# Kernel optimization log

Hardware: AMD Instinct MI355X
Metric: run time of the kernel (lower is better)

The kernel has to match this reference:

```python
import jax, jax.numpy as jnp
import numpy as np
import math

D_MODEL = 32    # channels; expand=1 => d_inner == d_model
D_STATE = 8
D_CONV = 4
DT_RANK = math.ceil(D_MODEL / 16)  # 2


def _layernorm(x, g, b, eps=1e-5):
    m = jnp.mean(x, axis=-1, keepdims=True)
    v = jnp.var(x, axis=-1, keepdims=True)
    return (x - m) * jax.lax.rsqrt(v + eps) * g + b


def _causal_dwconv(x, w, b):
    # x: [B, D, L], w: [D, 1, K] depthwise causal conv (pad K-1 on the left)
    y = jax.lax.conv_general_dilated(
        x, w, window_strides=(1,), padding=[(D_CONV - 1, 0)],
        dimension_numbers=('NCH', 'OIH', 'NCH'),
        feature_group_count=x.shape[1])
    return y + b[None, :, None]


def _ssm_branch(xb, z, conv_w, conv_b, xproj_w, dtproj_w, dtproj_b, A_log, Dp):
    # One mamba_inner (no out_proj) branch. xb, z: [B, D, L]
    Bsz, Dd, L = xb.shape
    u = jax.nn.silu(_causal_dwconv(xb, conv_w, conv_b))              # [B,D,L]
    x_dbl = jnp.einsum('bdl,rd->blr', u, xproj_w)                    # [B,L,R+2N]
    dt = x_dbl[..., :DT_RANK]                                        # [B,L,R]
    Bm = x_dbl[..., DT_RANK:DT_RANK + D_STATE]                       # [B,L,N]
    Cm = x_dbl[..., DT_RANK + D_STATE:]                              # [B,L,N]
    delta = jax.nn.softplus(jnp.einsum('blr,dr->bld', dt, dtproj_w) + dtproj_b)  # [B,L,D]
    A = -jnp.exp(A_log)                                              # [D,N]

    def step(h, inp):
        d_l, u_l, B_l, C_l = inp   # [B,D], [B,D], [B,N], [B,N]
        dA = jnp.exp(d_l[..., None] * A)                             # [B,D,N]
        h = dA * h + (d_l * u_l)[..., None] * B_l[:, None, :]
        y = jnp.einsum('bdn,bn->bd', h, C_l)
        return h, y

    h0 = jnp.zeros((Bsz, Dd, D_STATE), dtype=xb.dtype)
    _, ys = jax.lax.scan(step, h0,
                         (delta.transpose(1, 0, 2), u.transpose(2, 0, 1),
                          Bm.transpose(1, 0, 2), Cm.transpose(1, 0, 2)))
    y = ys.transpose(1, 2, 0)                                        # [B,D,L]
    y = y + Dp[None, :, None] * u
    return y * jax.nn.silu(z)


def _forward(x, w1, b1, ln_g, ln_b, in_proj_w,
             conv_w_f, conv_b_f, xproj_w_f, dtproj_w_f, dtproj_b_f, A_log_f, D_f,
             conv_w_b, conv_b_b, xproj_w_b, dtproj_w_b, dtproj_b_b, A_log_b, D_b,
             norm_g, norm_b, out_proj_w, w2, b2):
    s = jnp.max(x, axis=(2, 3))                                      # AdaptiveMaxPool2d((1,1)) -> [B,L]
    h = s[..., None] * w1[None, None, :, 0] + b1                     # Linear(1, d_model) -> [B,L,D]
    h = _layernorm(h, ln_g, ln_b)
    # Mamba, bimamba v2
    xz = jnp.einsum('bld,ed->bel', h, in_proj_w)                     # [B,2D,L]
    x_f, z_f = jnp.split(xz, 2, axis=1)
    out_f = _ssm_branch(x_f, z_f, conv_w_f, conv_b_f, xproj_w_f,
                        dtproj_w_f, dtproj_b_f, A_log_f, D_f)
    xz_r = jnp.flip(xz, axis=-1)
    x_b, z_b = jnp.split(xz_r, 2, axis=1)
    out_b = _ssm_branch(x_b, z_b, conv_w_b, conv_b_b, xproj_w_b,
                        dtproj_w_b, dtproj_b_b, A_log_b, D_b)
    y = (out_f + jnp.flip(out_b, axis=-1)).transpose(0, 2, 1)        # [B,L,D]
    y = _layernorm(y, norm_g, norm_b) / 2.0                          # use_norm + if_devide_out
    y = jnp.einsum('bld,od->blo', y, out_proj_w)                     # out_proj -> [B,L,D]
    o = jnp.einsum('bld,od->blo', y, w2) + b2                        # Linear(d_model, 1) -> [B,L,1]
    return jax.nn.sigmoid(o)[..., None]                              # [B,L,1,1]


def setup_inputs() -> dict:
    key = jax.random.key(0)
    ks = jax.random.split(key, 16)
    B, Cin, H, W = 16, 128, 256, 256
    D, N, R = D_MODEL, D_STATE, DT_RANK

    def nrm(k, shp, s=0.2):
        return jax.random.normal(k, shp, dtype=jnp.float32) * s

    A_log_init = jnp.log(jnp.arange(1, N + 1, dtype=jnp.float32))[None, :] * jnp.ones((D, 1), jnp.float32)
    return dict(
        x=jax.random.normal(ks[0], (B, Cin, H, W), dtype=jnp.float32),
        w1=nrm(ks[1], (D, 1), 0.5), b1=nrm(ks[2], (D,), 0.1),
        ln_g=jnp.ones((D,), jnp.float32), ln_b=jnp.zeros((D,), jnp.float32),
        in_proj_w=nrm(ks[3], (2 * D, D)),
        conv_w_f=nrm(ks[4], (D, 1, D_CONV)), conv_b_f=nrm(ks[5], (D,), 0.1),
        xproj_w_f=nrm(ks[6], (R + 2 * N, D)),
        dtproj_w_f=nrm(ks[7], (D, R)), dtproj_b_f=nrm(ks[8], (D,), 0.1),
        A_log_f=A_log_init, D_f=jnp.ones((D,), jnp.float32),
        conv_w_b=nrm(ks[9], (D, 1, D_CONV)), conv_b_b=nrm(ks[10], (D,), 0.1),
        xproj_w_b=nrm(ks[11], (R + 2 * N, D)),
        dtproj_w_b=nrm(ks[12], (D, R)), dtproj_b_b=nrm(ks[13], (D,), 0.1),
        A_log_b=A_log_init, D_b=jnp.ones((D,), jnp.float32),
        norm_g=jnp.ones((D,), jnp.float32), norm_b=jnp.zeros((D,), jnp.float32),
        out_proj_w=nrm(ks[14], (D, D)),
        w2=nrm(ks[15], (1, D), 0.5), b2=jnp.zeros((1,), jnp.float32),
    )


def reference(x, w1, b1, ln_g, ln_b, in_proj_w,
              conv_w_f, conv_b_f, xproj_w_f, dtproj_w_f, dtproj_b_f, A_log_f, D_f,
              conv_w_b, conv_b_b, xproj_w_b, dtproj_w_b, dtproj_b_b, A_log_b, D_b,
              norm_g, norm_b, out_proj_w, w2, b2):
    return _forward(x, w1, b1, ln_g, ln_b, in_proj_w,
                    conv_w_f, conv_b_f, xproj_w_f, dtproj_w_f, dtproj_b_f, A_log_f, D_f,
                    conv_w_b, conv_b_b, xproj_w_b, dtproj_w_b, dtproj_b_b, A_log_b, D_b,
                    norm_g, norm_b, out_proj_w, w2, b2)
```

## Files before the change

kernel.cpp:

```cpp
#include <hip/hip_runtime.h>
#include <hip/hip_bf16.h>
#include <math.h>

#define B_SZ 16
#define L_SEQ 128
#define D_M 32
#define HW 65536
#define NROWS (B_SZ * 128)
#define NCHUNK 2

typedef float vfloat4 __attribute__((ext_vector_type(4)));

__device__ float g_part[NROWS * NCHUNK];
__device__ float g_y[2][B_SZ * D_M * L_SEQ];
__device__ int   g_done[B_SZ];

__device__ __forceinline__ float silu_acc(float x) {
    return x / (1.f + __expf(-x));
}
__device__ __forceinline__ float softplusf(float x) {
    return (x > 20.f) ? x : log1pf(__expf(x));
}

__device__ __forceinline__ float row_max(int row) {
    const int r2 = row * NCHUNK;
    return fmaxf(g_part[r2], g_part[r2 + 1]);
}

__device__ __forceinline__ void compute_h(int row, const float* __restrict__ w1,
                                          const float* __restrict__ b1,
                                          const float* __restrict__ lng,
                                          const float* __restrict__ lnb,
                                          float h[D_M]) {
    const float s = row_max(row);
    float mean = 0.f;
#pragma unroll
    for (int d = 0; d < D_M; d++) { h[d] = s * w1[d] + b1[d]; mean += h[d]; }
    mean *= (1.f / D_M);
    float var = 0.f;
#pragma unroll
    for (int d = 0; d < D_M; d++) { float t = h[d] - mean; var += t * t; }
    var *= (1.f / D_M);
    const float rs = rsqrtf(var + 1e-5f);
#pragma unroll
    for (int d = 0; d < D_M; d++) h[d] = (h[d] - mean) * rs * lng[d] + lnb[d];
}

__global__ __launch_bounds__(256) void kmax(const float* __restrict__ x) {
    const int blk = blockIdx.x;
    const vfloat4* __restrict__ p =
        reinterpret_cast<const vfloat4*>(x) + (size_t)blk * 8192;
    const int t = threadIdx.x;
    float m0 = -INFINITY, m1 = -INFINITY, m2 = -INFINITY, m3 = -INFINITY;
#pragma unroll
    for (int i = 0; i < 8192; i += 1024) {
        vfloat4 v0 = __builtin_nontemporal_load(p + i + t);
        vfloat4 v1 = __builtin_nontemporal_load(p + i + t + 256);
        vfloat4 v2 = __builtin_nontemporal_load(p + i + t + 512);
        vfloat4 v3 = __builtin_nontemporal_load(p + i + t + 768);
        m0 = fmaxf(m0, fmaxf(fmaxf(v0.x, v0.y), fmaxf(v0.z, v0.w)));
        m1 = fmaxf(m1, fmaxf(fmaxf(v1.x, v1.y), fmaxf(v1.z, v1.w)));
        m2 = fmaxf(m2, fmaxf(fmaxf(v2.x, v2.y), fmaxf(v2.z, v2.w)));
        m3 = fmaxf(m3, fmaxf(fmaxf(v3.x, v3.y), fmaxf(v3.z, v3.w)));
    }
    float m = fmaxf(fmaxf(m0, m1), fmaxf(m2, m3));
#pragma unroll
    for (int off = 32; off >= 1; off >>= 1)
        m = fmaxf(m, __shfl_xor(m, off));
    __shared__ float sm[4];
    if ((threadIdx.x & 63) == 0) sm[threadIdx.x >> 6] = m;
    __syncthreads();
    if (threadIdx.x == 0)
        g_part[blk] = fmaxf(fmaxf(sm[0], sm[1]), fmaxf(sm[2], sm[3]));
}

__global__ __launch_bounds__(1024) void ktail(
    const float* __restrict__ w1,  const float* __restrict__ b1,
    const float* __restrict__ lng, const float* __restrict__ lnb,
    const float* __restrict__ Win,
    const float* __restrict__ cw_f, const float* __restrict__ cb_f,
    const float* __restrict__ xp_f, const float* __restrict__ dtw_f,
    const float* __restrict__ dtb_f, const float* __restrict__ Al_f,
    const float* __restrict__ Dp_f,
    const float* __restrict__ cw_b, const float* __restrict__ cb_b,
    const float* __restrict__ xp_b, const float* __restrict__ dtw_b,
    const float* __restrict__ dtb_b, const float* __restrict__ Al_b,
    const float* __restrict__ Dp_b,
    const float* __restrict__ ng,  const float* __restrict__ nb,
    const float* __restrict__ Wout, const float* __restrict__ w2,
    const float* __restrict__ b2,  float* __restrict__ out) {
    const int b   = blockIdx.x >> 1;
    const int dir = blockIdx.x & 1;
    const int tid = threadIdx.x;

    const float* cw  = dir ? cw_b  : cw_f;
    const float* cb  = dir ? cb_b  : cb_f;
    const float* xp  = dir ? xp_b  : xp_f;
    const float* dtw = dir ? dtw_b : dtw_f;
    const float* dtb = dir ? dtb_b : dtb_f;
    const float* Al  = dir ? Al_b  : Al_f;
    const float* Dp  = dir ? Dp_b  : Dp_f;

    __shared__ __align__(16) float S[15136];
    __shared__ int s_flag;
    float* sx  = S;
    float* sdl = S;
    float* su  = S + 4352;
    float* sy  = S + 8576;
    float* sdt = S + 12800;
    float* sB  = S + 13056;
    float* sC  = S + 14080;
    float* smm = S + 15104;

    const int l = tid & 127;
    const int q = tid >> 7;
    const int qq = __builtin_amdgcn_readfirstlane(q);

    if (tid < 128) sx[(tid >> 2) * 136 + (tid & 3)] = 0.f;
    if (tid >= 128 && tid < 160) {
        const int d = tid - 128;
        float mm = 0.f;
#pragma unroll
        for (int o = 0; o < D_M; o++) mm += w2[o] * Wout[o * 32 + d];
        smm[d] = mm;
    }
    float h[D_M];
    compute_h(b * L_SEQ + l, w1, b1, lng, lnb, h);

    {
        const int lw = dir ? (127 - l) : l;
#pragma unroll
        for (int k = 0; k < 4; k++) {
            const int e = qq * 4 + k;
            float acc = 0.f;
#pragma unroll
            for (int d = 0; d < D_M; d++) acc += h[d] * Win[e * 32 + d];
            sx[e * 136 + 4 + lw] = acc;
        }
    }

    float zs[4];
#pragma unroll
    for (int k = 0; k < 4; k++) {
        const int d = qq * 4 + k;
        float z = 0.f;
#pragma unroll
        for (int kk = 0; kk < D_M; kk++) z += h[kk] * Win[(32 + d) * 32 + kk];
        zs[k] = silu_acc(z);
    }
    __syncthreads();

    {
        const int d  = tid >> 5;
        const int l0 = (tid & 31) * 4;
        const vfloat4* px = reinterpret_cast<const vfloat4*>(sx + d * 136 + l0);
        vfloat4 a0 = px[0], a1 = px[1];
        float xv[7] = {a0.y, a0.z, a0.w, a1.x, a1.y, a1.z, a1.w};
        const float c0 = cw[d*4+0], c1 = cw[d*4+1], c2 = cw[d*4+2], c3 = cw[d*4+3];
        const float cbd = cb[d];
        float uo[4];
#pragma unroll
        for (int j = 0; j < 4; j++) {
            float acc = cbd + c0*xv[j] + c1*xv[j+1] + c2*xv[j+2] + c3*xv[j+3];
            uo[j] = silu_acc(acc);
        }
        vfloat4 u0 = {uo[0], uo[1], uo[2], uo[3]};
        *reinterpret_cast<vfloat4*>(su + d * 132 + l0) = u0;
    }
    __syncthreads();

    {
        float ul[D_M];
#pragma unroll
        for (int d = 0; d < D_M; d++) ul[d] = su[d * 132 + l];
#pragma unroll
        for (int rep = 0; rep < 3; rep++) {
            const int r = qq + rep * 8;
            if (rep == 2 && qq >= 2) break;
            float acc = 0.f;
#pragma unroll
            for (int d = 0; d < D_M; d++) acc += ul[d] * xp[r * 32 + d];
            if (r < 2)       sdt[l * 2 + r] = acc;
            else if (r < 10) sB[l * 8 + (r - 2)] = acc;
            else             sC[l * 8 + (r - 10)] = acc;
        }
    }
    __syncthreads();

    {
        const float dt0 = sdt[l * 2 + 0], dt1 = sdt[l * 2 + 1];
        const int d0 = qq * 4;
#pragma unroll
        for (int j = 0; j < 4; j++) {
            const int d = d0 + j;
            const float t = dt0 * dtw[d * 2 + 0] + dt1 * dtw[d * 2 + 1] + dtb[d];
            sdl[l * 33 + d] = softplusf(t);
        }
    }
    __syncthreads();

    if (tid < 256) {
        const int d = tid >> 3;
        const int c = tid & 7;
        float An[8];
        {
            const vfloat4* ap = reinterpret_cast<const vfloat4*>(Al + d * 8);
            vfloat4 a0 = ap[0], a1 = ap[1];
            An[0]=a0.x; An[1]=a0.y; An[2]=a0.z; An[3]=a0.w;
            An[4]=a1.x; An[5]=a1.y; An[6]=a1.z; An[7]=a1.w;
#pragma unroll
            for (int n = 0; n < 8; n++) An[n] = -__expf(An[n]);
        }
        const float Dd = Dp[d];
        const int lbase = c * 16;

        float Ap[8], Wp[8];
#pragma unroll
        for (int n = 0; n < 8; n++) { Ap[n] = 1.f; Wp[n] = 0.f; }
        for (int i = 0; i < 16; i++) {
            const int ll = lbase + i;
            const float dl = sdl[ll * 33 + d];
            const float ul = su[d * 132 + ll];
            const float du = dl * ul;
            const vfloat4* bp = reinterpret_cast<const vfloat4*>(sB + ll * 8);
            vfloat4 b0 = bp[0], b1 = bp[1];
            float Bv[8] = {b0.x,b0.y,b0.z,b0.w,b1.x,b1.y,b1.z,b1.w};
#pragma unroll
            for (int n = 0; n < 8; n++) {
                const float dA = __expf(dl * An[n]);
                Wp[n] = dA * Wp[n] + du * Bv[n];
                Ap[n] *= dA;
            }
        }
#pragma unroll
        for (int s = 1; s < 8; s <<= 1) {
#pragma unroll
            for (int n = 0; n < 8; n++) {
                const float Au = __shfl_up(Ap[n], s, 8);
                const float Wu = __shfl_up(Wp[n], s, 8);
                if (c >= s) {
                    Wp[n] = Ap[n] * Wu + Wp[n];
                    Ap[n] = Ap[n] * Au;
                }
            }
        }
        float hn[8];
#pragma unroll
        for (int n = 0; n < 8; n++) {
            const float Wu = __shfl_up(Wp[n], 1, 8);
            hn[n] = (c == 0) ? 0.f : Wu;
        }
        for (int i = 0; i < 16; i++) {
            const int ll = lbase + i;
            const float dl = sdl[ll * 33 + d];
            const float ul = su[d * 132 + ll];
            const float du = dl * ul;
            const vfloat4* bp = reinterpret_cast<const vfloat4*>(sB + ll * 8);
            const vfloat4* cp = reinterpret_cast<const vfloat4*>(sC + ll * 8);
            vfloat4 b0 = bp[0], b1 = bp[1];
            vfloat4 c0 = cp[0], c1 = cp[1];
            float Bv[8] = {b0.x,b0.y,b0.z,b0.w,b1.x,b1.y,b1.z,b1.w};
            float Cv[8] = {c0.x,c0.y,c0.z,c0.w,c1.x,c1.y,c1.z,c1.w};
            float y = 0.f;
#pragma unroll
            for (int n = 0; n < 8; n++) {
                const float dA = __expf(dl * An[n]);
                hn[n] = dA * hn[n] + du * Bv[n];
                y += hn[n] * Cv[n];
            }
            sy[d * 132 + ll] = y + Dd * ul;
        }
    }
    __syncthreads();

    for (int i = tid; i < 4096; i += 1024) {
        const int d = i >> 7, li = i & 127;
        const int gl = dir ? (127 - li) : li;
        g_y[dir][(b * D_M + d) * L_SEQ + gl] = sy[d * 132 + li];
    }
    __syncthreads();

    if (tid == 0) {
        __threadfence();
        const int old = atomicAdd(&g_done[b], 1);
        const int win = (old == 1);
        if (win) {
            atomicExch(&g_done[b], 0);
            __threadfence();
        }
        s_flag = win;
    }
    __syncthreads();
    if (!s_flag) return;

    {
        float* sv = S;
        const float* y0 = g_y[0] + (size_t)b * D_M * L_SEQ;
        const float* y1 = g_y[1] + (size_t)b * D_M * L_SEQ;

#pragma unroll
        for (int k = 0; k < 4; k++) {
            const int d = qq * 4 + k;
            const float yc = y0[d * L_SEQ + l] + y1[d * L_SEQ + l];
            sv[l * 33 + d] = yc * zs[k];
        }
        __syncthreads();

        if (tid < 128) {
            float vv[D_M];
            float mean = 0.f;
#pragma unroll
            for (int d = 0; d < D_M; d++) { vv[d] = sv[l * 33 + d]; mean += vv[d]; }
            mean *= (1.f / D_M);
            float var = 0.f;
#pragma unroll
            for (int d = 0; d < D_M; d++) { float t = vv[d] - mean; var += t * t; }
            var *= (1.f / D_M);
            const float rs = rsqrtf(var + 1e-5f);

            float acc = b2[0];
#pragma unroll
            for (int d = 0; d < D_M; d++) {
                const float y = ((vv[d] - mean) * rs * ng[d] + nb[d]) * 0.5f;
                acc += y * smm[d];
            }
            out[b * L_SEQ + l] = 1.f / (1.f + __expf(-acc));
        }
    }
}

extern "C" void kernel_launch(void* const* d_in, const int* in_sizes, int n_in,
                              void* d_out, int out_size, void* d_ws, size_t ws_size,
                              hipStream_t stream) {
    const float* x        = (const float*)d_in[0];
    const float* w1       = (const float*)d_in[1];
    const float* b1       = (const float*)d_in[2];
    const float* ln_g     = (const float*)d_in[3];
    const float* ln_b     = (const float*)d_in[4];
    const float* in_proj  = (const float*)d_in[5];
    const float* cw_f     = (const float*)d_in[6];
    const float* cb_f     = (const float*)d_in[7];
    const float* xp_f     = (const float*)d_in[8];
    const float* dtw_f    = (const float*)d_in[9];
    const float* dtb_f    = (const float*)d_in[10];
    const float* Al_f     = (const float*)d_in[11];
    const float* Dp_f     = (const float*)d_in[12];
    const float* cw_b     = (const float*)d_in[13];
    const float* cb_b     = (const float*)d_in[14];
    const float* xp_b     = (const float*)d_in[15];
    const float* dtw_b    = (const float*)d_in[16];
    const float* dtb_b    = (const float*)d_in[17];
    const float* Al_b     = (const float*)d_in[18];
    const float* Dp_b     = (const float*)d_in[19];
    const float* norm_g   = (const float*)d_in[20];
    const float* norm_b   = (const float*)d_in[21];
    const float* Wout     = (const float*)d_in[22];
    const float* w2       = (const float*)d_in[23];
    const float* b2       = (const float*)d_in[24];

    kmax<<<NROWS * NCHUNK, 256, 0, stream>>>(x);
    ktail<<<B_SZ * 2, 1024, 0, stream>>>(w1, b1, ln_g, ln_b, in_proj,
                                         cw_f, cb_f, xp_f, dtw_f, dtb_f, Al_f, Dp_f,
                                         cw_b, cb_b, xp_b, dtw_b, dtb_b, Al_b, Dp_b,
                                         norm_g, norm_b, Wout, w2, b2, (float*)d_out);
}
```

Measured before the change: 102.4 us.

## Fuse max-reduction and SSM tail into one kernel with per-batch counter handoff

Merges the row-max kernel and the per-batch SSM tail kernel into a single launch. Each of the 2048 blocks reduces one full row with 512 threads and bumps a per-batch atomic counter. The first two blocks of each batch then spin until all 128 rows of that batch are done and run the forward and backward scans, each thread now covering twice as many channels. This removes a kernel launch boundary and lets the tail overlap with reductions for other batches. The cost is a spin-wait that relies on those blocks being co-resident, plus fewer threads and more registers per thread in the tail.

```diff
diff --git a/kernel.cpp b/kernel.cpp
--- a/kernel.cpp
+++ b/kernel.cpp
@@ -6,13 +6,12 @@
 #define L_SEQ 128
 #define D_M 32
 #define HW 65536
-#define NROWS (B_SZ * 128)
-#define NCHUNK 2
 
 typedef float vfloat4 __attribute__((ext_vector_type(4)));
 
-__device__ float g_part[NROWS * NCHUNK];
+__device__ float g_part[B_SZ * L_SEQ];
 __device__ float g_y[2][B_SZ * D_M * L_SEQ];
+__device__ int   g_cnt[B_SZ];
 __device__ int   g_done[B_SZ];
 
 __device__ __forceinline__ float silu_acc(float x) {
@@ -22,59 +21,8 @@
     return (x > 20.f) ? x : log1pf(__expf(x));
 }
 
-__device__ __forceinline__ float row_max(int row) {
-    const int r2 = row * NCHUNK;
-    return fmaxf(g_part[r2], g_part[r2 + 1]);
-}
-
-__device__ __forceinline__ void compute_h(int row, const float* __restrict__ w1,
-                                          const float* __restrict__ b1,
-                                          const float* __restrict__ lng,
-                                          const float* __restrict__ lnb,
-                                          float h[D_M]) {
-    const float s = row_max(row);
-    float mean = 0.f;
-#pragma unroll
-    for (int d = 0; d < D_M; d++) { h[d] = s * w1[d] + b1[d]; mean += h[d]; }
-    mean *= (1.f / D_M);
-    float var = 0.f;
-#pragma unroll
-    for (int d = 0; d < D_M; d++) { float t = h[d] - mean; var += t * t; }
-    var *= (1.f / D_M);
-    const float rs = rsqrtf(var + 1e-5f);
-#pragma unroll
-    for (int d = 0; d < D_M; d++) h[d] = (h[d] - mean) * rs * lng[d] + lnb[d];
-}
-
-__global__ __launch_bounds__(256) void kmax(const float* __restrict__ x) {
-    const int blk = blockIdx.x;
-    const vfloat4* __restrict__ p =
-        reinterpret_cast<const vfloat4*>(x) + (size_t)blk * 8192;
-    const int t = threadIdx.x;
-    float m0 = -INFINITY, m1 = -INFINITY, m2 = -INFINITY, m3 = -INFINITY;
-#pragma unroll
-    for (int i = 0; i < 8192; i += 1024) {
-        vfloat4 v0 = __builtin_nontemporal_load(p + i + t);
-        vfloat4 v1 = __builtin_nontemporal_load(p + i + t + 256);
-        vfloat4 v2 = __builtin_nontemporal_load(p + i + t + 512);
-        vfloat4 v3 = __builtin_nontemporal_load(p + i + t + 768);
-        m0 = fmaxf(m0, fmaxf(fmaxf(v0.x, v0.y), fmaxf(v0.z, v0.w)));
-        m1 = fmaxf(m1, fmaxf(fmaxf(v1.x, v1.y), fmaxf(v1.z, v1.w)));
-        m2 = fmaxf(m2, fmaxf(fmaxf(v2.x, v2.y), fmaxf(v2.z, v2.w)));
-        m3 = fmaxf(m3, fmaxf(fmaxf(v3.x, v3.y), fmaxf(v3.z, v3.w)));
-    }
-    float m = fmaxf(fmaxf(m0, m1), fmaxf(m2, m3));
-#pragma unroll
-    for (int off = 32; off >= 1; off >>= 1)
-        m = fmaxf(m, __shfl_xor(m, off));
-    __shared__ float sm[4];
-    if ((threadIdx.x & 63) == 0) sm[threadIdx.x >> 6] = m;
-    __syncthreads();
-    if (threadIdx.x == 0)
-        g_part[blk] = fmaxf(fmaxf(sm[0], sm[1]), fmaxf(sm[2], sm[3]));
-}
-
-__global__ __launch_bounds__(1024) void ktail(
+__global__ __launch_bounds__(512) void fused(
+    const float* __restrict__ x,
     const float* __restrict__ w1,  const float* __restrict__ b1,
     const float* __restrict__ lng, const float* __restrict__ lnb,
     const float* __restrict__ Win,
@@ -89,9 +37,52 @@
     const float* __restrict__ ng,  const float* __restrict__ nb,
     const float* __restrict__ Wout, const float* __restrict__ w2,
     const float* __restrict__ b2,  float* __restrict__ out) {
-    const int b   = blockIdx.x >> 1;
-    const int dir = blockIdx.x & 1;
+    const int row = blockIdx.x;
+    const int b   = row >> 7;
     const int tid = threadIdx.x;
+
+    __shared__ __align__(16) float S[15136];
+    __shared__ float s_m[8];
+    __shared__ int s_flag;
+
+    {
+        const vfloat4* __restrict__ p =
+            reinterpret_cast<const vfloat4*>(x) + (size_t)row * 16384;
+        float m0 = -INFINITY, m1 = -INFINITY, m2 = -INFINITY, m3 = -INFINITY;
+#pragma unroll
+        for (int i = 0; i < 16384; i += 2048) {
+            vfloat4 v0 = __builtin_nontemporal_load(p + i + tid);
+            vfloat4 v1 = __builtin_nontemporal_load(p + i + tid + 512);
+            vfloat4 v2 = __builtin_nontemporal_load(p + i + tid + 1024);
+            vfloat4 v3 = __builtin_nontemporal_load(p + i + tid + 1536);
+            m0 = fmaxf(m0, fmaxf(fmaxf(v0.x, v0.y), fmaxf(v0.z, v0.w)));
+            m1 = fmaxf(m1, fmaxf(fmaxf(v1.x, v1.y), fmaxf(v1.z, v1.w)));
+            m2 = fmaxf(m2, fmaxf(fmaxf(v2.x, v2.y), fmaxf(v2.z, v2.w)));
+            m3 = fmaxf(m3, fmaxf(fmaxf(v3.x, v3.y), fmaxf(v3.z, v3.w)));
+        }
+        float m = fmaxf(fmaxf(m0, m1), fmaxf(m2, m3));
+#pragma unroll
+        for (int off = 32; off >= 1; off >>= 1)
+            m = fmaxf(m, __shfl_xor(m, off));
+        if ((tid & 63) == 0) s_m[tid >> 6] = m;
+        __syncthreads();
+        if (tid == 0) {
+            float mm = s_m[0];
+#pragma unroll
+            for (int w = 1; w < 8; w++) mm = fmaxf(mm, s_m[w]);
+            g_part[row] = mm;
+            __threadfence();
+            atomicAdd(&g_cnt[b], 1);
+        }
+    }
+    if ((row & 127) >= 2) return;
+
+    const int dir = row & 1;
+    if (tid == 0) {
+        while (atomicAdd(&g_cnt[b], 0) < 128) __builtin_amdgcn_s_sleep(8);
+        __threadfence();
+    }
+    __syncthreads();
 
     const float* cw  = dir ? cw_b  : cw_f;
     const float* cb  = dir ? cb_b  : cb_f;
@@ -101,8 +92,6 @@
     const float* Al  = dir ? Al_b  : Al_f;
     const float* Dp  = dir ? Dp_b  : Dp_f;
 
-    __shared__ __align__(16) float S[15136];
-    __shared__ int s_flag;
     float* sx  = S;
     float* sdl = S;
     float* su  = S + 4352;
@@ -125,13 +114,26 @@
         smm[d] = mm;
     }
     float h[D_M];
-    compute_h(b * L_SEQ + l, w1, b1, lng, lnb, h);
+    {
+        const float s = g_part[b * L_SEQ + l];
+        float mean = 0.f;
+#pragma unroll
+        for (int d = 0; d < D_M; d++) { h[d] = s * w1[d] + b1[d]; mean += h[d]; }
+        mean *= (1.f / D_M);
+        float var = 0.f;
+#pragma unroll
+        for (int d = 0; d < D_M; d++) { float t = h[d] - mean; var += t * t; }
+        var *= (1.f / D_M);
+        const float rs = rsqrtf(var + 1e-5f);
+#pragma unroll
+        for (int d = 0; d < D_M; d++) h[d] = (h[d] - mean) * rs * lng[d] + lnb[d];
+    }
 
     {
         const int lw = dir ? (127 - l) : l;
 #pragma unroll
-        for (int k = 0; k < 4; k++) {
-            const int e = qq * 4 + k;
+        for (int k = 0; k < 8; k++) {
+            const int e = qq * 8 + k;
             float acc = 0.f;
 #pragma unroll
             for (int d = 0; d < D_M; d++) acc += h[d] * Win[e * 32 + d];
@@ -139,10 +141,10 @@
         }
     }
 
-    float zs[4];
-#pragma unroll
-    for (int k = 0; k < 4; k++) {
-        const int d = qq * 4 + k;
+    float zs[8];
+#pragma unroll
+    for (int k = 0; k < 8; k++) {
+        const int d = qq * 8 + k;
         float z = 0.f;
 #pragma unroll
         for (int kk = 0; kk < D_M; kk++) z += h[kk] * Win[(32 + d) * 32 + kk];
@@ -151,21 +153,22 @@
     __syncthreads();
 
     {
-        const int d  = tid >> 5;
-        const int l0 = (tid & 31) * 4;
+        const int d  = tid >> 4;
+        const int l0 = (tid & 15) * 8;
         const vfloat4* px = reinterpret_cast<const vfloat4*>(sx + d * 136 + l0);
-        vfloat4 a0 = px[0], a1 = px[1];
-        float xv[7] = {a0.y, a0.z, a0.w, a1.x, a1.y, a1.z, a1.w};
+        vfloat4 a0 = px[0], a1 = px[1], a2 = px[2];
+        float xv[12] = {a0.x,a0.y,a0.z,a0.w, a1.x,a1.y,a1.z,a1.w, a2.x,a2.y,a2.z,a2.w};
         const float c0 = cw[d*4+0], c1 = cw[d*4+1], c2 = cw[d*4+2], c3 = cw[d*4+3];
         const float cbd = cb[d];
-        float uo[4];
-#pragma unroll
-        for (int j = 0; j < 4; j++) {
-            float acc = cbd + c0*xv[j] + c1*xv[j+1] + c2*xv[j+2] + c3*xv[j+3];
+        float uo[8];
+#pragma unroll
+        for (int j = 0; j < 8; j++) {
+            float acc = cbd + c0*xv[j+1] + c1*xv[j+2] + c2*xv[j+3] + c3*xv[j+4];
             uo[j] = silu_acc(acc);
         }
-        vfloat4 u0 = {uo[0], uo[1], uo[2], uo[3]};
-        *reinterpret_cast<vfloat4*>(su + d * 132 + l0) = u0;
+        vfloat4 u0 = {uo[0],uo[1],uo[2],uo[3]}, u1 = {uo[4],uo[5],uo[6],uo[7]};
+        vfloat4* pu = reinterpret_cast<vfloat4*>(su + d * 132 + l0);
+        pu[0] = u0; pu[1] = u1;
     }
     __syncthreads();
 
@@ -174,9 +177,9 @@
 #pragma unroll
         for (int d = 0; d < D_M; d++) ul[d] = su[d * 132 + l];
 #pragma unroll
-        for (int rep = 0; rep < 3; rep++) {
-            const int r = qq + rep * 8;
-            if (rep == 2 && qq >= 2) break;
+        for (int rep = 0; rep < 5; rep++) {
+            const int r = qq + rep * 4;
+            if (rep == 4 && qq >= 2) break;
             float acc = 0.f;
 #pragma unroll
             for (int d = 0; d < D_M; d++) acc += ul[d] * xp[r * 32 + d];
@@ -189,9 +192,9 @@
 
     {
         const float dt0 = sdt[l * 2 + 0], dt1 = sdt[l * 2 + 1];
-        const int d0 = qq * 4;
-#pragma unroll
-        for (int j = 0; j < 4; j++) {
+        const int d0 = qq * 8;
+#pragma unroll
+        for (int j = 0; j < 8; j++) {
             const int d = d0 + j;
             const float t = dt0 * dtw[d * 2 + 0] + dt1 * dtw[d * 2 + 1] + dtb[d];
             sdl[l * 33 + d] = softplusf(t);
@@ -273,7 +276,7 @@
     }
     __syncthreads();
 
-    for (int i = tid; i < 4096; i += 1024) {
+    for (int i = tid; i < 4096; i += 512) {
         const int d = i >> 7, li = i & 127;
         const int gl = dir ? (127 - li) : li;
         g_y[dir][(b * D_M + d) * L_SEQ + gl] = sy[d * 132 + li];
@@ -291,16 +294,15 @@
         s_flag = win;
     }
     __syncthreads();
-    if (!s_flag) return;
-
-    {
+
+    if (s_flag) {
         float* sv = S;
         const float* y0 = g_y[0] + (size_t)b * D_M * L_SEQ;
         const float* y1 = g_y[1] + (size_t)b * D_M * L_SEQ;
 
 #pragma unroll
-        for (int k = 0; k < 4; k++) {
-            const int d = qq * 4 + k;
+        for (int k = 0; k < 8; k++) {
+            const int d = qq * 8 + k;
             const float yc = y0[d * L_SEQ + l] + y1[d * L_SEQ + l];
             sv[l * 33 + d] = yc * zs[k];
         }
@@ -326,6 +328,12 @@
             }
             out[b * L_SEQ + l] = 1.f / (1.f + __expf(-acc));
         }
+        __syncthreads();
+    }
+
+    if (tid == 0) {
+        const int old = atomicAdd(&g_cnt[b], 1);
+        if (old == 129) atomicExch(&g_cnt[b], 0);
     }
 }
 
@@ -358,9 +366,9 @@
     const float* w2       = (const float*)d_in[23];
     const float* b2       = (const float*)d_in[24];
 
-    kmax<<<NROWS * NCHUNK, 256, 0, stream>>>(x);
-    ktail<<<B_SZ * 2, 1024, 0, stream>>>(w1, b1, ln_g, ln_b, in_proj,
-                                         cw_f, cb_f, xp_f, dtw_f, dtb_f, Al_f, Dp_f,
-                                         cw_b, cb_b, xp_b, dtw_b, dtb_b, Al_b, Dp_b,
-                                         norm_g, norm_b, Wout, w2, b2, (float*)d_out);
+    fused<<<B_SZ * L_SEQ, 512, 0, stream>>>(
+        x, w1, b1, ln_g, ln_b, in_proj,
+        cw_f, cb_f, xp_f, dtw_f, dtb_f, Al_f, Dp_f,
+        cw_b, cb_b, xp_b, dtw_b, dtb_b, Al_b, Dp_b,
+        norm_g, norm_b, Wout, w2, b2, (float*)d_out);
 }
```

Result: slower. 222.9 us (+117.7%).
